# Kernel optimization log

Measured on AMD Instinct MI355X. Metric: run time of the kernel, lower is better.

The kernel has to match this reference:

```python
import jax, jax.numpy as jnp
import numpy as np

HEADS = 8
N_STATE = 512
MAX_SEQ = 2048
DEPTH = N_STATE // HEADS
EPS = 1e-5


def layer_norm(x, g, b):
    mu = jnp.mean(x, axis=-1, keepdims=True)
    var = jnp.mean(jnp.square(x - mu), axis=-1, keepdims=True)
    return (x - mu) * jax.lax.rsqrt(var + EPS) * g + b


def setup_inputs() -> dict:
    key = jax.random.key(0)
    ks = jax.random.split(key, 12)
    B, S = 2, 2048
    x = jax.random.normal(ks[0], (B, S, N_STATE), dtype=jnp.float32)
    # causal additive mask (upper triangle = -1e9)
    mask = jnp.where(jnp.tril(jnp.ones((S, S), dtype=bool)), 0.0, -1e9).astype(jnp.float32)
    sc = 0.02
    Wqkv = jax.random.normal(ks[1], (N_STATE, 3 * N_STATE), dtype=jnp.float32) * sc
    bqkv = jnp.zeros((3 * N_STATE,), dtype=jnp.float32)
    Wproj = jax.random.normal(ks[2], (N_STATE, N_STATE), dtype=jnp.float32) * sc
    bproj = jnp.zeros((N_STATE,), dtype=jnp.float32)
    # xavier-normal-ish relative position embeddings, shape (H, max_seq, depth)
    E = jax.random.normal(ks[3], (HEADS, MAX_SEQ, DEPTH), dtype=jnp.float32) * (2.0 / (MAX_SEQ + DEPTH)) ** 0.5
    g1 = jnp.ones((N_STATE,), dtype=jnp.float32)
    b1 = jnp.zeros((N_STATE,), dtype=jnp.float32)
    g2 = jnp.ones((N_STATE,), dtype=jnp.float32)
    b2 = jnp.zeros((N_STATE,), dtype=jnp.float32)
    W1 = jax.random.normal(ks[4], (N_STATE, 4 * N_STATE), dtype=jnp.float32) * sc
    bm1 = jnp.zeros((4 * N_STATE,), dtype=jnp.float32)
    W2 = jax.random.normal(ks[5], (4 * N_STATE, N_STATE), dtype=jnp.float32) * sc
    bm2 = jnp.zeros((N_STATE,), dtype=jnp.float32)
    return {"x": x, "mask": mask, "Wqkv": Wqkv, "bqkv": bqkv, "Wproj": Wproj,
            "bproj": bproj, "E": E, "g1": g1, "b1": b1, "g2": g2, "b2": b2,
            "W1": W1, "bm1": bm1, "W2": W2, "bm2": bm2}


def relative_attn(q, E):
    # q: [B,H,S,D]; E: [H,max_seq,D] -> rel: [B,H,S,S] via skew trick
    B, H, S, D = q.shape
    Es = E[:, MAX_SEQ - S:]                      # [H,S,D]
    rel = jnp.einsum('bhsd,htd->bhst', q, Es)    # [B,H,S,S]
    rel = jnp.pad(rel, ((0, 0), (0, 0), (0, 0), (1, 0)))  # pad left of last dim
    rel = rel.reshape(B, H, S + 1, S)[:, :, 1:]  # skew: drop first row
    return rel


def reference(x, mask, Wqkv, bqkv, Wproj, bproj, E, g1, b1, g2, b2, W1, bm1, W2, bm2):
    B, S, _ = x.shape
    # --- attention sublayer ---
    a = layer_norm(x, g1, b1)
    qkv = a @ Wqkv + bqkv                        # [B,S,3*n_state]
    q, k, v = jnp.split(qkv, 3, axis=-1)
    def heads(t):
        return t.reshape(B, S, HEADS, DEPTH).transpose(0, 2, 1, 3)  # [B,H,S,D]
    q, k, v = heads(q), heads(k), heads(v)
    w = jnp.einsum('bhsd,bhtd->bhst', q, k) + relative_attn(q, E)
    w = w * (1.0 / jnp.sqrt(jnp.float32(DEPTH)))
    w = w + mask                                  # broadcast [S,S]
    w = jax.nn.softmax(w, axis=-1)
    att = jnp.einsum('bhst,bhtd->bhsd', w, v)
    att = att.transpose(0, 2, 1, 3).reshape(B, S, N_STATE)
    att = att @ Wproj + bproj
    x = x + att
    # --- MLP sublayer ---
    m = layer_norm(x, g2, b2)
    m = jax.nn.gelu(m @ W1 + bm1) @ W2 + bm2
    return x + m
```

## Files before the change

kernel.cpp:

```cpp
#include <hip/hip_runtime.h>
#include <math.h>

typedef unsigned short u16;
typedef unsigned int u32;
using short8 = __attribute__((ext_vector_type(8))) short;
using f32x4  = __attribute__((ext_vector_type(4))) float;

#define SEQ 2048
#define NH 8
#define DM 512
#define DH 64
#define NROWS 4096
#define BATCH 2
#define KVB 128

__device__ __forceinline__ float bf2f(u16 u) {
  union { u32 i; float f; } c; c.i = ((u32)u) << 16; return c.f;
}
__device__ __forceinline__ u16 f2bf(float f) {
  union { float f; u32 i; } c; c.f = f;
  u32 r = c.i + 0x7fffu + ((c.i >> 16) & 1u);
  return (u16)(r >> 16);
}

__device__ __forceinline__ void gll16(const u16* g, u16* l) {
  __builtin_amdgcn_global_load_lds(
      (const __attribute__((address_space(1))) u32*)g,
      (__attribute__((address_space(3))) u32*)l, 16, 0, 0);
}

template<int N> __device__ __forceinline__ void waitcnt_vm() {
  if constexpr (N == 0)      asm volatile("s_waitcnt vmcnt(0)" ::: "memory");
  else if constexpr (N == 4) asm volatile("s_waitcnt vmcnt(4)" ::: "memory");
  else if constexpr (N == 6) asm volatile("s_waitcnt vmcnt(6)" ::: "memory");
  else if constexpr (N == 8) asm volatile("s_waitcnt vmcnt(8)" ::: "memory");
}

__global__ __launch_bounds__(64) void ln_bf16_kernel(
    const float* __restrict__ x, const float* __restrict__ gw,
    const float* __restrict__ bw, u16* __restrict__ out)
{
  int row = blockIdx.x;
  int lane = threadIdx.x;
  const float* xr = x + (size_t)row * DM;
  float4 v0 = ((const float4*)xr)[lane];
  float4 v1 = ((const float4*)xr)[lane + 64];
  float s  = v0.x + v0.y + v0.z + v0.w + v1.x + v1.y + v1.z + v1.w;
  float s2 = v0.x*v0.x + v0.y*v0.y + v0.z*v0.z + v0.w*v0.w
           + v1.x*v1.x + v1.y*v1.y + v1.z*v1.z + v1.w*v1.w;
  #pragma unroll
  for (int m = 1; m < 64; m <<= 1) {
    s  += __shfl_xor(s,  m);
    s2 += __shfl_xor(s2, m);
  }
  float mu   = s * (1.0f / DM);
  float var  = s2 * (1.0f / DM) - mu * mu;
  float rstd = rsqrtf(var + 1e-5f);
  float4 ga = ((const float4*)gw)[lane],      ba = ((const float4*)bw)[lane];
  float4 gb = ((const float4*)gw)[lane + 64], bb = ((const float4*)bw)[lane + 64];
  ushort4 o0, o1;
  o0.x = f2bf((v0.x - mu) * rstd * ga.x + ba.x);
  o0.y = f2bf((v0.y - mu) * rstd * ga.y + ba.y);
  o0.z = f2bf((v0.z - mu) * rstd * ga.z + ba.z);
  o0.w = f2bf((v0.w - mu) * rstd * ga.w + ba.w);
  o1.x = f2bf((v1.x - mu) * rstd * gb.x + bb.x);
  o1.y = f2bf((v1.y - mu) * rstd * gb.y + bb.y);
  o1.z = f2bf((v1.z - mu) * rstd * gb.z + bb.z);
  o1.w = f2bf((v1.w - mu) * rstd * gb.w + bb.w);
  *(ushort4*)&out[(size_t)row * DM + lane * 4]       = o0;
  *(ushort4*)&out[(size_t)row * DM + 256 + lane * 4] = o1;
}

__global__ __launch_bounds__(256) void transpose_cast_kernel(
    const float* __restrict__ W, u16* __restrict__ Wt, int K, int N)
{
  __shared__ float tile[32][33];
  int bn = blockIdx.x * 32, bk = blockIdx.y * 32;
  int tx = threadIdx.x & 31, ty = threadIdx.x >> 5;
  #pragma unroll
  for (int i = 0; i < 32; i += 8)
    tile[ty + i][tx] = W[(size_t)(bk + ty + i) * N + bn + tx];
  __syncthreads();
  #pragma unroll
  for (int i = 0; i < 32; i += 8)
    Wt[(size_t)(bn + ty + i) * K + bk + tx] = f2bf(tile[tx][ty + i]);
}

__global__ __launch_bounds__(256) void cast_bf16_kernel(
    const float* __restrict__ in, u16* __restrict__ out, int n)
{
  int i = (blockIdx.x * 256 + threadIdx.x) * 4;
  if (i >= n) return;
  float4 v = *(const float4*)&in[i];
  ushort4 o;
  o.x = f2bf(v.x); o.y = f2bf(v.y); o.z = f2bf(v.z); o.w = f2bf(v.w);
  *(ushort4*)&out[i] = o;
}

template<int TM, int TN, int MODE>
__global__ __launch_bounds__(256) void gemm_bf16(
    const u16* __restrict__ A, const u16* __restrict__ Bt,
    const float* __restrict__ bias, const float* __restrict__ res,
    float* __restrict__ outF, u16* __restrict__ outB0,
    u16* __restrict__ outB1, u16* __restrict__ outB2,
    int M, int N, int K)
{
  constexpr int MI = TM / 32;
  constexpr int NI = TN / 32;
  constexpr int LOADS = TM / 32 + TN / 32;
  __shared__ u16 sA[2][TM * 64];
  __shared__ u16 sB[2][TN * 64];
  int tid = threadIdx.x;
  int lane = tid & 63, wv = tid >> 6;
  int wm = wv >> 1, wn = wv & 1;
  int g = lane >> 4, l15 = lane & 15;

  int nwg = gridDim.x, lin = blockIdx.x;
  int qq = nwg >> 3;
  int wg = (lin & 7) * qq + (lin >> 3);
  int ntn = N / TN;
  int m0 = (wg / ntn) * TM, n0 = (wg % ntn) * TN;

  auto stage = [&](int buf, int k0) {
    #pragma unroll
    for (int s = 0; s < TM / 32; ++s) {
      int c = s * 256 + tid;
      int row = c >> 3, p = c & 7;
      gll16(&A[(size_t)(m0 + row) * K + k0 + ((p ^ (row & 7)) * 8)],
            &sA[buf][(size_t)(s * 256 + wv * 64) * 8]);
    }
    #pragma unroll
    for (int s = 0; s < TN / 32; ++s) {
      int c = s * 256 + tid;
      int row = c >> 3, p = c & 7;
      gll16(&Bt[(size_t)(n0 + row) * K + k0 + ((p ^ (row & 7)) * 8)],
            &sB[buf][(size_t)(s * 256 + wv * 64) * 8]);
    }
  };

  f32x4 acc[MI][NI] = {};
  stage(0, 0);

  int nk = K / 64;
  for (int kt = 0; kt < nk; ++kt) {
    int cur = kt & 1;
    __syncthreads();
    if (kt + 1 < nk) {
      stage(cur ^ 1, (kt + 1) * 64);
      waitcnt_vm<LOADS>();
    } else {
      waitcnt_vm<0>();
    }
    __syncthreads();
    #pragma unroll
    for (int kk = 0; kk < 2; ++kk) {
      short8 af[MI], bfr[NI];
      #pragma unroll
      for (int i = 0; i < MI; ++i) {
        int row = wm * (TM / 2) + i * 16 + l15;
        af[i] = *(const short8*)&sA[cur][row * 64 + (((4 * kk + g) ^ (row & 7)) * 8)];
      }
      #pragma unroll
      for (int i = 0; i < NI; ++i) {
        int row = wn * (TN / 2) + i * 16 + l15;
        bfr[i] = *(const short8*)&sB[cur][row * 64 + (((4 * kk + g) ^ (row & 7)) * 8)];
      }
      #pragma unroll
      for (int mi = 0; mi < MI; ++mi)
        #pragma unroll
        for (int ni = 0; ni < NI; ++ni)
          acc[mi][ni] = __builtin_amdgcn_mfma_f32_16x16x32_bf16(af[mi], bfr[ni], acc[mi][ni], 0, 0, 0);
    }
  }

  #pragma unroll
  for (int mi = 0; mi < MI; ++mi) {
    #pragma unroll
    for (int ni = 0; ni < NI; ++ni) {
      #pragma unroll
      for (int r = 0; r < 4; ++r) {
        int grow = m0 + wm * (TM / 2) + mi * 16 + g * 4 + r;
        int gcol = n0 + wn * (TN / 2) + ni * 16 + l15;
        float val = acc[mi][ni][r] + bias[gcol];
        if (MODE == 0) {
          int part = gcol >> 9, c = gcol & 511;
          int hh = c >> 6, dd = c & 63;
          int bb = grow >> 11, ss = grow & 2047;
          size_t dst = (((size_t)(bb * NH + hh)) * SEQ + ss) * DH + dd;
          if (part == 0)      outB0[dst] = f2bf(val * 0.18033688011112042f);
          else if (part == 1) outB1[dst] = f2bf(val);
          else                outB2[dst] = f2bf(val);
        } else if (MODE == 1 || MODE == 3) {
          size_t idx = (size_t)grow * DM + gcol;
          outF[idx] = val + res[idx];
        } else {
          float t = val;
          float inner = 0.7978845608028654f * (t + 0.044715f * t * t * t);
          float gl = 0.5f * t * (1.0f + tanhf(inner));
          outB0[(size_t)grow * N + gcol] = f2bf(gl);
        }
      }
    }
  }
}

__global__ __launch_bounds__(256, 2) void attn_kernel(
    const u16* __restrict__ Q, const u16* __restrict__ Kb,
    const u16* __restrict__ Vb, const u16* __restrict__ Eb,
    u16* __restrict__ Ob)
{
  __shared__ u16 sK[KVB * 64];
  __shared__ u16 sV[64 * (KVB + 8)];
  __shared__ u16 sP[4][16 * 64];
  __shared__ float sM[2][32];
  __shared__ float sS[2][32];

  int tid = threadIdx.x, lane = tid & 63, wv = tid >> 6;
  int wr = wv & 1, wc = wv >> 1;
  int g = lane >> 4, l15 = lane & 15;
  int lin = blockIdx.x;
  int bh   = (lin & 7) * 2 + ((lin >> 3) & 1);
  int tile = 63 - (lin >> 4);
  int hh = bh & (NH - 1), bb = bh >> 3;
  int NIT = tile / 4 + 1;

  const u16* Qh = Q  + (size_t)bh * SEQ * DH;
  const u16* Kh = Kb + (size_t)bh * SEQ * DH;
  const u16* Vh = Vb + (size_t)bh * SEQ * DH;
  const u16* Eh = Eb + (size_t)hh * SEQ * DH;

  int rstage = tid >> 3, cstage = (tid & 7) * 8;

  #pragma unroll
  for (int s = 0; s < 4; ++s) {
    int c = s * 256 + tid, t = c >> 3, pc = c & 7;
    gll16(&Kh[(size_t)t * DH + ((pc ^ (t & 7)) * 8)],
          &sK[(size_t)(s * 256 + wv * 64) * 8]);
  }
  #pragma unroll
  for (int q = 0; q < 4; ++q) {
    int t = q * 32 + rstage;
    short8 vv = *(const short8*)&Vh[(size_t)t * DH + cstage];
    #pragma unroll
    for (int j = 0; j < 8; ++j) {
      int d = cstage + j;
      sV[d * (KVB + 8) + (((t >> 3) ^ (d >> 3)) * 8) + (t & 7)] = (u16)vv[j];
    }
  }
  asm volatile("s_waitcnt vmcnt(0)" ::: "memory");
  __syncthreads();

  int sw = tile * 32 + wr * 16;
  short8 qf[2];
  qf[0] = *(const short8*)&Qh[(size_t)(sw + l15) * DH + g * 8];
  qf[1] = *(const short8*)&Qh[(size_t)(sw + l15) * DH + g * 8 + 32];

  f32x4 o[4] = {};
  float mrow[4] = {-1e30f, -1e30f, -1e30f, -1e30f};
  float lsum[4] = {};

  float* sO = (float*)&sP[0][0];

  for (int it = 0; it < NIT; ++it) {
    int t0 = it * KVB;
    bool pre = (it + 1 < NIT);
    int tb = (it + 1) * KVB;

    short8 vp[4];
    if (pre) {
      #pragma unroll
      for (int q = 0; q < 4; ++q)
        vp[q] = *(const short8*)&Vh[(size_t)(tb + q * 32 + rstage) * DH + cstage];
    }

    f32x4 accS[4];
    #pragma unroll
    for (int ni = 0; ni < 4; ++ni) {
      int row = wc * 64 + ni * 16 + l15;
      short8 k0 = *(const short8*)&sK[row * 64 + ((g ^ (row & 7)) * 8)];
      short8 k1 = *(const short8*)&sK[row * 64 + (((4 + g) ^ (row & 7)) * 8)];
      f32x4 z = {};
      z = __builtin_amdgcn_mfma_f32_16x16x32_bf16(qf[0], k0, z, 0, 0, 0);
      z = __builtin_amdgcn_mfma_f32_16x16x32_bf16(qf[1], k1, z, 0, 0, 0);
      accS[ni] = z;
    }

    int jbase = 2032 - sw + t0 + wc * 64;
    f32x4 accR[5];
    #pragma unroll
    for (int nb = 0; nb < 5; ++nb) {
      int j = jbase + nb * 16 + l15; if (j > 2047) j = 2047;
      short8 e0 = *(const short8*)&Eh[(size_t)j * DH + g * 8];
      short8 e1 = *(const short8*)&Eh[(size_t)j * DH + 32 + g * 8];
      f32x4 z = {};
      z = __builtin_amdgcn_mfma_f32_16x16x32_bf16(qf[0], e0, z, 0, 0, 0);
      z = __builtin_amdgcn_mfma_f32_16x16x32_bf16(qf[1], e1, z, 0, 0, 0);
      accR[nb] = z;
    }

    bool needMask = (t0 + wc * 64 + 63 > sw);
    #pragma unroll
    for (int r = 0; r < 4; ++r) {
      int srow = g * 4 + r;
      int dsh = 15 - srow + l15;
      int srcl = (lane & 48) + (dsh & 15);
      float sh[5];
      #pragma unroll
      for (int nb = 0; nb < 5; ++nb) sh[nb] = __shfl(accR[nb][r], srcl);
      bool cy = dsh >= 16;
      #pragma unroll
      for (int ni = 0; ni < 4; ++ni) {
        float rel = cy ? sh[ni + 1] : sh[ni];
        float val = accS[ni][r] + rel;
        if (needMask && (t0 + wc * 64 + ni * 16 + l15 > sw + srow)) val = -1e30f;
        accS[ni][r] = val;
      }
    }

    float lmax[4];
    #pragma unroll
    for (int r = 0; r < 4; ++r) {
      float tm = fmaxf(fmaxf(accS[0][r], accS[1][r]), fmaxf(accS[2][r], accS[3][r]));
      tm = fmaxf(tm, __shfl_xor(tm, 1));
      tm = fmaxf(tm, __shfl_xor(tm, 2));
      tm = fmaxf(tm, __shfl_xor(tm, 4));
      tm = fmaxf(tm, __shfl_xor(tm, 8));
      lmax[r] = tm;
    }
    if (l15 == 0) {
      #pragma unroll
      for (int r = 0; r < 4; ++r) sM[wc][wr * 16 + g * 4 + r] = lmax[r];
    }
    __syncthreads();
    if (pre) {
      #pragma unroll
      for (int s = 0; s < 4; ++s) {
        int c = s * 256 + tid, t = c >> 3, pc = c & 7;
        gll16(&Kh[(size_t)(tb + t) * DH + ((pc ^ (t & 7)) * 8)],
              &sK[(size_t)(s * 256 + wv * 64) * 8]);
      }
    }
    float4 om = *(float4*)&sM[wc ^ 1][wr * 16 + g * 4];

    float sesav[4], lscl[4];
    #pragma unroll
    for (int r = 0; r < 4; ++r) {
      float gm = fmaxf(lmax[r], ((float*)&om)[r]);
      float mnew = fmaxf(mrow[r], gm);
      lscl[r] = exp2f(mrow[r] - mnew);
      mrow[r] = mnew;
      float se = 0.f;
      #pragma unroll
      for (int ni = 0; ni < 4; ++ni) {
        float pe = exp2f(accS[ni][r] - mnew);
        accS[ni][r] = pe;
        se += pe;
      }
      se += __shfl_xor(se, 1); se += __shfl_xor(se, 2);
      se += __shfl_xor(se, 4); se += __shfl_xor(se, 8);
      sesav[r] = se;
      o[0][r] *= lscl[r]; o[1][r] *= lscl[r]; o[2][r] *= lscl[r]; o[3][r] *= lscl[r];
    }
    if (l15 == 0) {
      #pragma unroll
      for (int r = 0; r < 4; ++r) sS[wc][wr * 16 + g * 4 + r] = sesav[r];
    }

    #pragma unroll
    for (int ni = 0; ni < 4; ++ni)
      #pragma unroll
      for (int r = 0; r < 4; ++r) {
        int srow = g * 4 + r;
        int chunk = (ni * 2 + (l15 >> 3)) ^ (srow & 7);
        sP[wv][srow * 64 + chunk * 8 + (l15 & 7)] = f2bf(accS[ni][r]);
      }
    asm volatile("s_waitcnt lgkmcnt(0)" ::: "memory");
    __builtin_amdgcn_sched_barrier(0);
    #pragma unroll
    for (int kk = 0; kk < 2; ++kk) {
      short8 pf = *(const short8*)&sP[wv][l15 * 64 + (((kk * 4 + g) ^ (l15 & 7)) * 8)];
      #pragma unroll
      for (int nb = 0; nb < 4; ++nb) {
        int d = nb * 16 + l15;
        int ck = wc * 8 + kk * 4 + g;
        short8 vf = *(const short8*)&sV[d * (KVB + 8) + ((ck ^ (d >> 3)) * 8)];
        o[nb] = __builtin_amdgcn_mfma_f32_16x16x32_bf16(pf, vf, o[nb], 0, 0, 0);
      }
    }

    __syncthreads();
    float4 os = *(float4*)&sS[wc ^ 1][wr * 16 + g * 4];
    #pragma unroll
    for (int r = 0; r < 4; ++r)
      lsum[r] = lsum[r] * lscl[r] + sesav[r] + ((float*)&os)[r];

    if (pre) {
      #pragma unroll
      for (int q = 0; q < 4; ++q) {
        int t = q * 32 + rstage;
        #pragma unroll
        for (int j = 0; j < 8; ++j) {
          int d = cstage + j;
          sV[d * (KVB + 8) + (((t >> 3) ^ (d >> 3)) * 8) + (t & 7)] = (u16)vp[q][j];
        }
      }
    }
  }

  {
    if (wc == 1) {
      #pragma unroll
      for (int r = 0; r < 4; ++r) {
        float rl = 1.0f / lsum[r];
        #pragma unroll
        for (int nb = 0; nb < 4; ++nb)
          sO[wr * 1024 + (g * 4 + r) * 64 + nb * 16 + l15] = o[nb][r] * rl;
      }
    }
    __syncthreads();
    if (wc == 0) {
      #pragma unroll
      for (int r = 0; r < 4; ++r) {
        float rl = 1.0f / lsum[r];
        int ss = sw + g * 4 + r;
        #pragma unroll
        for (int nb = 0; nb < 4; ++nb) {
          float val = o[nb][r] * rl + sO[wr * 1024 + (g * 4 + r) * 64 + nb * 16 + l15];
          Ob[((size_t)(bb * SEQ + ss)) * DM + hh * DH + nb * 16 + l15] = f2bf(val);
        }
      }
    }
  }
}

extern "C" void kernel_launch(void* const* d_in, const int* in_sizes, int n_in,
                              void* d_out, int out_size, void* d_ws, size_t ws_size,
                              hipStream_t stream) {
  const float* x     = (const float*)d_in[0];
  const float* Wqkv  = (const float*)d_in[2];
  const float* bqkv  = (const float*)d_in[3];
  const float* Wproj = (const float*)d_in[4];
  const float* bproj = (const float*)d_in[5];
  const float* E     = (const float*)d_in[6];
  const float* g1    = (const float*)d_in[7];
  const float* b1    = (const float*)d_in[8];
  const float* g2    = (const float*)d_in[9];
  const float* b2    = (const float*)d_in[10];
  const float* W1    = (const float*)d_in[11];
  const float* bm1   = (const float*)d_in[12];
  const float* W2    = (const float*)d_in[13];
  const float* bm2   = (const float*)d_in[14];
  float* out = (float*)d_out;

  char* ws = (char*)d_ws;
  size_t off = 0;
  auto alloc = [&](size_t bytes) {
    void* p = ws + off;
    off += (bytes + 255) & ~(size_t)255;
    return p;
  };
  u16* a_bf   = (u16*)alloc((size_t)NROWS * DM * 2);
  u16* q_bf   = (u16*)alloc((size_t)NROWS * DM * 2);
  u16* k_bf   = (u16*)alloc((size_t)NROWS * DM * 2);
  u16* v_bf   = (u16*)alloc((size_t)NROWS * DM * 2);
  u16* att_bf = (u16*)alloc((size_t)NROWS * DM * 2);
  float* y    = (float*)alloc((size_t)NROWS * DM * 4);
  u16* h_bf   = (u16*)alloc((size_t)NROWS * 2048 * 2);
  u16* WqkvT  = (u16*)alloc((size_t)1536 * 512 * 2);
  u16* WprojT = (u16*)alloc((size_t)512 * 512 * 2);
  u16* W1T    = (u16*)alloc((size_t)2048 * 512 * 2);
  u16* W2T    = (u16*)alloc((size_t)512 * 2048 * 2);
  u16* E_bf   = (u16*)alloc((size_t)NH * SEQ * DH * 2);

  transpose_cast_kernel<<<dim3(1536 / 32, 512 / 32), 256, 0, stream>>>(Wqkv, WqkvT, 512, 1536);
  transpose_cast_kernel<<<dim3(512 / 32, 512 / 32), 256, 0, stream>>>(Wproj, WprojT, 512, 512);
  transpose_cast_kernel<<<dim3(2048 / 32, 512 / 32), 256, 0, stream>>>(W1, W1T, 512, 2048);
  transpose_cast_kernel<<<dim3(512 / 32, 2048 / 32), 256, 0, stream>>>(W2, W2T, 2048, 512);
  cast_bf16_kernel<<<(NH * SEQ * DH) / (256 * 4), 256, 0, stream>>>(E, E_bf, NH * SEQ * DH);

  ln_bf16_kernel<<<NROWS, 64, 0, stream>>>(x, g1, b1, a_bf);
  gemm_bf16<64, 128, 0><<<(NROWS / 64) * (1536 / 128), 256, 0, stream>>>(
      a_bf, WqkvT, bqkv, nullptr, nullptr, q_bf, k_bf, v_bf, NROWS, 1536, 512);
  attn_kernel<<<1024, 256, 0, stream>>>(q_bf, k_bf, v_bf, E_bf, att_bf);
  gemm_bf16<64, 64, 1><<<(NROWS / 64) * (512 / 64), 256, 0, stream>>>(
      att_bf, WprojT, bproj, x, y, nullptr, nullptr, nullptr, NROWS, 512, 512);
  ln_bf16_kernel<<<NROWS, 64, 0, stream>>>(y, g2, b2, a_bf);
  gemm_bf16<64, 128, 2><<<(NROWS / 64) * (2048 / 128), 256, 0, stream>>>(
      a_bf, W1T, bm1, nullptr, nullptr, h_bf, nullptr, nullptr, NROWS, 2048, 512);
  gemm_bf16<64, 64, 3><<<(NROWS / 64) * (512 / 64), 256, 0, stream>>>(
      h_bf, W2T, bm2, y, out, nullptr, nullptr, nullptr, NROWS, 512, 2048);
}
```

Measured before the change: 168.1 us.

## Keep independent per-wave softmax state and merge the two KV halves at the end

Each of the two column-waves now keeps its own running max and sum over its half of the KV tile, instead of swapping row maxima and sums through shared memory every iteration. The two partial results are combined once after the loop with a flash-decoding style rescale. This removes the per-iteration LDS exchange and one dependency on a barrier. The K prefetch is moved earlier, right after the QK MFMAs, behind a new barrier. The running max now starts at -64 instead of -1e30, which changes behaviour for rows whose scores are all masked in the early tiles and relies on exp2 underflow to keep those masked entries from contributing.

After: 171.0 us. Within noise of the previous version (+1.7%).

```diff
diff --git a/kernel.cpp b/kernel.cpp
--- a/kernel.cpp
+++ b/kernel.cpp
@@ -256,7 +256,7 @@
   qf[1] = *(const short8*)&Qh[(size_t)(sw + l15) * DH + g * 8 + 32];
 
   f32x4 o[4] = {};
-  float mrow[4] = {-1e30f, -1e30f, -1e30f, -1e30f};
+  float mrow[4] = {-64.f, -64.f, -64.f, -64.f};
   float lsum[4] = {};
 
   float* sO = (float*)&sP[0][0];
@@ -285,6 +285,16 @@
       accS[ni] = z;
     }
 
+    __syncthreads();
+    if (pre) {
+      #pragma unroll
+      for (int s = 0; s < 4; ++s) {
+        int c = s * 256 + tid, t = c >> 3, pc = c & 7;
+        gll16(&Kh[(size_t)(tb + t) * DH + ((pc ^ (t & 7)) * 8)],
+              &sK[(size_t)(s * 256 + wv * 64) * 8]);
+      }
+    }
+
     int jbase = 2032 - sw + t0 + wc * 64;
     f32x4 accR[5];
     #pragma unroll
@@ -317,7 +327,6 @@
       }
     }
 
-    float lmax[4];
     #pragma unroll
     for (int r = 0; r < 4; ++r) {
       float tm = fmaxf(fmaxf(accS[0][r], accS[1][r]), fmaxf(accS[2][r], accS[3][r]));
@@ -325,29 +334,8 @@
       tm = fmaxf(tm, __shfl_xor(tm, 2));
       tm = fmaxf(tm, __shfl_xor(tm, 4));
       tm = fmaxf(tm, __shfl_xor(tm, 8));
-      lmax[r] = tm;
-    }
-    if (l15 == 0) {
-      #pragma unroll
-      for (int r = 0; r < 4; ++r) sM[wc][wr * 16 + g * 4 + r] = lmax[r];
-    }
-    __syncthreads();
-    if (pre) {
-      #pragma unroll
-      for (int s = 0; s < 4; ++s) {
-        int c = s * 256 + tid, t = c >> 3, pc = c & 7;
-        gll16(&Kh[(size_t)(tb + t) * DH + ((pc ^ (t & 7)) * 8)],
-              &sK[(size_t)(s * 256 + wv * 64) * 8]);
-      }
-    }
-    float4 om = *(float4*)&sM[wc ^ 1][wr * 16 + g * 4];
-
-    float sesav[4], lscl[4];
-    #pragma unroll
-    for (int r = 0; r < 4; ++r) {
-      float gm = fmaxf(lmax[r], ((float*)&om)[r]);
-      float mnew = fmaxf(mrow[r], gm);
-      lscl[r] = exp2f(mrow[r] - mnew);
+      float mnew = fmaxf(mrow[r], tm);
+      float scl = exp2f(mrow[r] - mnew);
       mrow[r] = mnew;
       float se = 0.f;
       #pragma unroll
@@ -358,12 +346,8 @@
       }
       se += __shfl_xor(se, 1); se += __shfl_xor(se, 2);
       se += __shfl_xor(se, 4); se += __shfl_xor(se, 8);
-      sesav[r] = se;
-      o[0][r] *= lscl[r]; o[1][r] *= lscl[r]; o[2][r] *= lscl[r]; o[3][r] *= lscl[r];
-    }
-    if (l15 == 0) {
-      #pragma unroll
-      for (int r = 0; r < 4; ++r) sS[wc][wr * 16 + g * 4 + r] = sesav[r];
+      lsum[r] = lsum[r] * scl + se;
+      o[0][r] *= scl; o[1][r] *= scl; o[2][r] *= scl; o[3][r] *= scl;
     }
 
     #pragma unroll
@@ -389,10 +373,6 @@
     }
 
     __syncthreads();
-    float4 os = *(float4*)&sS[wc ^ 1][wr * 16 + g * 4];
-    #pragma unroll
-    for (int r = 0; r < 4; ++r)
-      lsum[r] = lsum[r] * lscl[r] + sesav[r] + ((float*)&os)[r];
 
     if (pre) {
       #pragma unroll
@@ -408,24 +388,41 @@
   }
 
   {
+    if (l15 == 0) {
+      #pragma unroll
+      for (int r = 0; r < 4; ++r) {
+        sM[wc][wr * 16 + g * 4 + r] = mrow[r];
+        sS[wc][wr * 16 + g * 4 + r] = lsum[r];
+      }
+    }
+    __syncthreads();
+    float4 om = *(float4*)&sM[wc ^ 1][wr * 16 + g * 4];
+    float4 ol = *(float4*)&sS[wc ^ 1][wr * 16 + g * 4];
+    float fac[4];
+    #pragma unroll
+    for (int r = 0; r < 4; ++r) {
+      float mg = fmaxf(mrow[r], ((float*)&om)[r]);
+      float w  = exp2f(mrow[r] - mg);
+      float wo = exp2f(((float*)&om)[r] - mg);
+      float den = lsum[r] * w + ((float*)&ol)[r] * wo;
+      fac[r] = w / den;
+    }
+    __syncthreads();
     if (wc == 1) {
       #pragma unroll
-      for (int r = 0; r < 4; ++r) {
-        float rl = 1.0f / lsum[r];
+      for (int r = 0; r < 4; ++r)
         #pragma unroll
         for (int nb = 0; nb < 4; ++nb)
-          sO[wr * 1024 + (g * 4 + r) * 64 + nb * 16 + l15] = o[nb][r] * rl;
-      }
+          sO[wr * 1024 + (g * 4 + r) * 64 + nb * 16 + l15] = o[nb][r] * fac[r];
     }
     __syncthreads();
     if (wc == 0) {
       #pragma unroll
       for (int r = 0; r < 4; ++r) {
-        float rl = 1.0f / lsum[r];
         int ss = sw + g * 4 + r;
         #pragma unroll
         for (int nb = 0; nb < 4; ++nb) {
-          float val = o[nb][r] * rl + sO[wr * 1024 + (g * 4 + r) * 64 + nb * 16 + l15];
+          float val = o[nb][r] * fac[r] + sO[wr * 1024 + (g * 4 + r) * 64 + nb * 16 + l15];
           Ob[((size_t)(bb * SEQ + ss)) * DM + hh * DH + nb * 16 + l15] = f2bf(val);
         }
       }
```

## Store V transposed from QKV GEMM and double-buffer V via async LDS loads

Applied to the files above, without the earlier changes.

The QKV GEMM epilogue now writes V in a [B,H,D,S] transposed layout. This lets the attention kernel stage V tiles with direct global-to-LDS 16-byte loads into a swizzled, double-buffered shared array. It replaces the register prefetch followed by a scalar 8-way scatter transpose into LDS. That removes many LDS store instructions and frees registers, at the cost of doubling V's LDS footprint. The GEMM now writes V in strided scattered form, which may hurt that kernel's store coalescing.

After: 168.7 us. Within noise of the previous version (+0.4%).

```diff
diff --git a/kernel.cpp b/kernel.cpp
--- a/kernel.cpp
+++ b/kernel.cpp
@@ -186,10 +186,16 @@
           int part = gcol >> 9, c = gcol & 511;
           int hh = c >> 6, dd = c & 63;
           int bb = grow >> 11, ss = grow & 2047;
-          size_t dst = (((size_t)(bb * NH + hh)) * SEQ + ss) * DH + dd;
-          if (part == 0)      outB0[dst] = f2bf(val * 0.18033688011112042f);
-          else if (part == 1) outB1[dst] = f2bf(val);
-          else                outB2[dst] = f2bf(val);
+          if (part == 0) {
+            size_t dst = (((size_t)(bb * NH + hh)) * SEQ + ss) * DH + dd;
+            outB0[dst] = f2bf(val * 0.18033688011112042f);
+          } else if (part == 1) {
+            size_t dst = (((size_t)(bb * NH + hh)) * SEQ + ss) * DH + dd;
+            outB1[dst] = f2bf(val);
+          } else {
+            size_t dst = (((size_t)(bb * NH + hh)) * DH + dd) * SEQ + ss;
+            outB2[dst] = f2bf(val);
+          }
         } else if (MODE == 1 || MODE == 3) {
           size_t idx = (size_t)grow * DM + gcol;
           outF[idx] = val + res[idx];
@@ -210,7 +216,7 @@
     u16* __restrict__ Ob)
 {
   __shared__ u16 sK[KVB * 64];
-  __shared__ u16 sV[64 * (KVB + 8)];
+  __shared__ u16 sVt[2][64 * KVB];
   __shared__ u16 sP[4][16 * 64];
   __shared__ float sM[2][32];
   __shared__ float sS[2][32];
@@ -226,10 +232,18 @@
 
   const u16* Qh = Q  + (size_t)bh * SEQ * DH;
   const u16* Kh = Kb + (size_t)bh * SEQ * DH;
-  const u16* Vh = Vb + (size_t)bh * SEQ * DH;
+  const u16* Vt = Vb + (size_t)bh * DH * SEQ;
   const u16* Eh = Eb + (size_t)hh * SEQ * DH;
 
-  int rstage = tid >> 3, cstage = (tid & 7) * 8;
+  int vrow = tid >> 4;
+  int vsrc = ((tid & 15) ^ vrow) * 8;
+  auto stageV = [&](int buf, int tb) {
+    #pragma unroll
+    for (int s = 0; s < 4; ++s) {
+      gll16(&Vt[(size_t)(s * 16 + vrow) * SEQ + tb + vsrc],
+            &sVt[buf][(size_t)(s * 256 + wv * 64) * 8]);
+    }
+  };
 
   #pragma unroll
   for (int s = 0; s < 4; ++s) {
@@ -237,16 +251,7 @@
     gll16(&Kh[(size_t)t * DH + ((pc ^ (t & 7)) * 8)],
           &sK[(size_t)(s * 256 + wv * 64) * 8]);
   }
-  #pragma unroll
-  for (int q = 0; q < 4; ++q) {
-    int t = q * 32 + rstage;
-    short8 vv = *(const short8*)&Vh[(size_t)t * DH + cstage];
-    #pragma unroll
-    for (int j = 0; j < 8; ++j) {
-      int d = cstage + j;
-      sV[d * (KVB + 8) + (((t >> 3) ^ (d >> 3)) * 8) + (t & 7)] = (u16)vv[j];
-    }
-  }
+  stageV(0, 0);
   asm volatile("s_waitcnt vmcnt(0)" ::: "memory");
   __syncthreads();
 
@@ -262,16 +267,9 @@
   float* sO = (float*)&sP[0][0];
 
   for (int it = 0; it < NIT; ++it) {
-    int t0 = it * KVB;
+    int t0 = it * KVB, cur = it & 1;
     bool pre = (it + 1 < NIT);
     int tb = (it + 1) * KVB;
-
-    short8 vp[4];
-    if (pre) {
-      #pragma unroll
-      for (int q = 0; q < 4; ++q)
-        vp[q] = *(const short8*)&Vh[(size_t)(tb + q * 32 + rstage) * DH + cstage];
-    }
 
     f32x4 accS[4];
     #pragma unroll
@@ -339,6 +337,7 @@
         gll16(&Kh[(size_t)(tb + t) * DH + ((pc ^ (t & 7)) * 8)],
               &sK[(size_t)(s * 256 + wv * 64) * 8]);
       }
+      stageV(cur ^ 1, tb);
     }
     float4 om = *(float4*)&sM[wc ^ 1][wr * 16 + g * 4];
 
@@ -381,9 +380,9 @@
       short8 pf = *(const short8*)&sP[wv][l15 * 64 + (((kk * 4 + g) ^ (l15 & 7)) * 8)];
       #pragma unroll
       for (int nb = 0; nb < 4; ++nb) {
-        int d = nb * 16 + l15;
+        int row = nb * 16 + l15;
         int ck = wc * 8 + kk * 4 + g;
-        short8 vf = *(const short8*)&sV[d * (KVB + 8) + ((ck ^ (d >> 3)) * 8)];
+        short8 vf = *(const short8*)&sVt[cur][row * KVB + ((ck ^ l15) * 8)];
         o[nb] = __builtin_amdgcn_mfma_f32_16x16x32_bf16(pf, vf, o[nb], 0, 0, 0);
       }
     }
@@ -393,18 +392,6 @@
     #pragma unroll
     for (int r = 0; r < 4; ++r)
       lsum[r] = lsum[r] * lscl[r] + sesav[r] + ((float*)&os)[r];
-
-    if (pre) {
-      #pragma unroll
-      for (int q = 0; q < 4; ++q) {
-        int t = q * 32 + rstage;
-        #pragma unroll
-        for (int j = 0; j < 8; ++j) {
-          int d = cstage + j;
-          sV[d * (KVB + 8) + (((t >> 3) ^ (d >> 3)) * 8) + (t & 7)] = (u16)vp[q][j];
-        }
-      }
-    }
   }
 
   {
```
